# Optimization experiments

Measured on AMD Instinct MI355X. Metric: run time of the kernel, lower is better.

Reference implementation:

```python
import jax, jax.numpy as jnp
import numpy as np

D_MODEL = 1024
N_HEADS = 16
L = 2048
S = 2048
B = 4


def setup_inputs() -> dict:
    key = jax.random.key(0)
    ks = jax.random.split(key, 12)
    std = 0.02
    inp = {
        "query": jax.random.normal(ks[0], (L, B, D_MODEL), dtype=jnp.float32),
        "key": jax.random.normal(ks[1], (S, B, D_MODEL), dtype=jnp.float32),
        "value": jax.random.normal(ks[2], (S, B, D_MODEL), dtype=jnp.float32),
        # True = masked (matches torch masked_fill semantics); causal mask
        "attn_mask": jnp.triu(jnp.ones((L, S), dtype=bool), k=1),
        "Wq": std * jax.random.normal(ks[3], (D_MODEL, D_MODEL), dtype=jnp.float32),
        "bq": jnp.zeros((D_MODEL,), dtype=jnp.float32),
        "Wk": std * jax.random.normal(ks[4], (D_MODEL, D_MODEL), dtype=jnp.float32),
        "bk": jnp.zeros((D_MODEL,), dtype=jnp.float32),
        "Wv": std * jax.random.normal(ks[5], (D_MODEL, D_MODEL), dtype=jnp.float32),
        "bv": jnp.zeros((D_MODEL,), dtype=jnp.float32),
        "Wo": std * jax.random.normal(ks[6], (D_MODEL, D_MODEL), dtype=jnp.float32),
        "bo": jnp.zeros((D_MODEL,), dtype=jnp.float32),
    }
    return inp


def reference(query, key, value, attn_mask, Wq, bq, Wk, bk, Wv, bv, Wo, bo):
    Lq, Bb, D = query.shape
    H = N_HEADS
    dh = D // H
    # NOTE: module uses d_model**-0.5 (not d_qkv**-0.5)
    scale = D ** (-0.5)
    Q = (query @ Wq.T + bq).reshape(Lq, Bb, H, dh)
    K = (key @ Wk.T + bk).reshape(-1, Bb, H, dh)
    V = (value @ Wv.T + bv).reshape(-1, Bb, H, dh)
    # scores: (L, S, B, H)
    scores = jnp.einsum('ibnd,jbnd->ijbn', Q, K) * scale
    scores = jnp.where(attn_mask[:, :, None, None], -jnp.inf, scores)
    attn_weights = jax.nn.softmax(scores, axis=1)  # softmax over key axis j
    # dropout in eval mode -> identity
    out = jnp.einsum('ijbn,jbnd->ibnd', attn_weights, V).reshape(Lq, Bb, D)
    out = out @ Wo.T + bo
    return out
```

## Files before the change

kernel.cpp:

```cpp
#include <hip/hip_runtime.h>
#include <hip/hip_bf16.h>

typedef __hip_bfloat16 bf16;
typedef __attribute__((ext_vector_type(8))) short short8;
typedef __attribute__((ext_vector_type(8))) __bf16 bf16x8;
typedef __attribute__((ext_vector_type(4))) float f32x4;
typedef __attribute__((ext_vector_type(2))) unsigned int u32x2;

#define L_CTX 2048
#define B_SZ 4
#define DM 1024
#define NH 16
#define DH 64
#define M_ROWS (L_CTX * B_SZ)
#define SCQ 0.04508422002778011f

__device__ __forceinline__ void load_lds16(const void* g, void* l) {
  __builtin_amdgcn_global_load_lds(
      (const __attribute__((address_space(1))) unsigned int*)g,
      (__attribute__((address_space(3))) unsigned int*)l, 16, 0, 0);
}

__device__ __forceinline__ f32x4 mfma16(short8 a, short8 b, f32x4 c) {
  return __builtin_amdgcn_mfma_f32_16x16x32_bf16(
      __builtin_bit_cast(bf16x8, a), __builtin_bit_cast(bf16x8, b), c, 0, 0, 0);
}

__device__ __forceinline__ short tobf(float x) {
  return __builtin_bit_cast(short, __float2bfloat16(x));
}

__device__ __forceinline__ short tobf_rh(float x) {
  unsigned u = __builtin_bit_cast(unsigned, x);
  return (short)((u + 0x8000u) >> 16);
}

#if __has_builtin(__builtin_amdgcn_exp2f)
#define EXP2(x) __builtin_amdgcn_exp2f(x)
#else
#define EXP2(x) exp2f(x)
#endif

#if __has_builtin(__builtin_amdgcn_rcpf)
#define RCP(x) __builtin_amdgcn_rcpf(x)
#else
#define RCP(x) (1.0f / (x))
#endif

#define TRRD(d, N) \
  asm volatile("ds_read_b64_tr_b16 %0, %1 offset:" #N : "=v"(d) : "v"(va))

__device__ __forceinline__ short8 mkv(u32x2 a, u32x2 b) {
  union { unsigned u[4]; short8 s; } x;
  x.u[0] = a.x; x.u[1] = a.y; x.u[2] = b.x; x.u[3] = b.y;
  return x.s;
}

__global__ void cast_all(const float* __restrict__ q, const float* __restrict__ k,
                         const float* __restrict__ v, const float* __restrict__ wq,
                         const float* __restrict__ wk, const float* __restrict__ wv,
                         const float* __restrict__ wo, bf16* __restrict__ dq,
                         bf16* __restrict__ dk, bf16* __restrict__ dv,
                         bf16* __restrict__ dwq, bf16* __restrict__ dwk,
                         bf16* __restrict__ dwv, bf16* __restrict__ dwo) {
  unsigned u = blockIdx.x * 256u + threadIdx.x;
  const float* src;
  bf16* dst;
  unsigned off;
  if (u < 3145728u) {
    unsigned which = u >> 20;
    off = u & 1048575u;
    src = which == 0 ? q : which == 1 ? k : v;
    dst = which == 0 ? dq : which == 1 ? dk : dv;
  } else {
    unsigned w = u - 3145728u;
    unsigned which = w >> 17;
    off = w & 131071u;
    src = which == 0 ? wq : which == 1 ? wk : which == 2 ? wv : wo;
    dst = which == 0 ? dwq : which == 1 ? dwk : which == 2 ? dwv : dwo;
  }
  const float4* s4 = (const float4*)src + (size_t)off * 2;
  float4 a = s4[0], b = s4[1];
  union { bf16 h[8]; short8 s; } o;
  o.h[0] = __float2bfloat16(a.x); o.h[1] = __float2bfloat16(a.y);
  o.h[2] = __float2bfloat16(a.z); o.h[3] = __float2bfloat16(a.w);
  o.h[4] = __float2bfloat16(b.x); o.h[5] = __float2bfloat16(b.y);
  o.h[6] = __float2bfloat16(b.z); o.h[7] = __float2bfloat16(b.w);
  *(short8*)(dst + (size_t)off * 8) = o.s;
}

__global__ __launch_bounds__(512, 2) void gemm_qkv(
    const bf16* __restrict__ Aq, const bf16* __restrict__ Ak,
    const bf16* __restrict__ Av, const bf16* __restrict__ Wq,
    const bf16* __restrict__ Wk, const bf16* __restrict__ Wv,
    const float* __restrict__ bq, const float* __restrict__ bk,
    const float* __restrict__ bv, bf16* __restrict__ Oq, bf16* __restrict__ Ok,
    bf16* __restrict__ Ov) {
  const int K = DM;
  int bid = blockIdx.x;
  int xcd = bid & 7, t_ = bid >> 3;
  int z = t_ >> 4, rem = t_ & 15;
  int bx = rem & 3, by = xcd * 4 + (rem >> 2);
  const bf16* A = z == 0 ? Aq : z == 1 ? Ak : Av;
  const bf16* W = z == 0 ? Wq : z == 1 ? Wk : Wv;
  const float* bias = z == 0 ? bq : z == 1 ? bk : bv;
  bf16* Cout = z == 0 ? Oq : z == 1 ? Ok : Ov;
  const float scale = z == 0 ? SCQ : 1.0f;

  const int tid = threadIdx.x;
  const int wid = tid >> 6, ln = tid & 63, g = ln >> 4, lc = ln & 15;
  const int wm = wid >> 2, wn = wid & 3;
  const int bm = by * 256, bn = bx * 256;

  __shared__ char smem[65536];

  f32x4 acc[8][4] = {};

  auto stage = [&](int t, int s) {
    int kk = t * 32;
#pragma unroll
    for (int l = 0; l < 4; ++l) {
      int idx = (l & 1) * 512 + tid;
      int rowi = idx >> 2, chunk = idx & 3;
      int cs = chunk ^ ((rowi >> 1) & 3);
      char* dst = smem + s * 32768 + (l >> 1) * 16384 + (l & 1) * 8192 +
                  wid * 1024 + ln * 16;
      if (l < 2)
        load_lds16(A + (size_t)(bm + rowi) * K + kk + cs * 8, dst);
      else
        load_lds16(W + (size_t)(bn + rowi) * K + kk + cs * 8, dst);
    }
  };

  stage(0, 0);
  asm volatile("s_waitcnt vmcnt(0)" ::: "memory");
  __syncthreads();

  for (int t = 0; t < 32; ++t) {
    if (t + 1 < 32) stage(t + 1, (t + 1) & 1);
    const char* As = smem + (t & 1) * 32768;
    const char* Bs = As + 16384;
    short8 af[8], bfr[4];
#pragma unroll
    for (int m = 0; m < 8; ++m) {
      int row = wm * 128 + m * 16 + lc;
      af[m] = *(const short8*)(As + row * 64 + ((g ^ ((row >> 1) & 3)) << 4));
    }
#pragma unroll
    for (int n = 0; n < 4; ++n) {
      int row = wn * 64 + n * 16 + lc;
      bfr[n] = *(const short8*)(Bs + row * 64 + ((g ^ ((row >> 1) & 3)) << 4));
    }
    __builtin_amdgcn_s_setprio(1);
#pragma unroll
    for (int m = 0; m < 8; ++m)
#pragma unroll
      for (int n = 0; n < 4; ++n) acc[m][n] = mfma16(af[m], bfr[n], acc[m][n]);
    __builtin_amdgcn_s_setprio(0);
    asm volatile("s_waitcnt vmcnt(0)" ::: "memory");
    __syncthreads();
  }

#pragma unroll
  for (int n = 0; n < 4; ++n) {
    int col = bn + wn * 64 + n * 16 + lc;
    float bv = bias[col];
    int h = col >> 6, d = col & 63;
#pragma unroll
    for (int m = 0; m < 8; ++m) {
      int row0 = bm + wm * 128 + m * 16 + g * 4;
#pragma unroll
      for (int i = 0; i < 4; ++i) {
        int row = row0 + i;
        int l = row >> 2, b = row & 3;
        Cout[(((size_t)(b * NH + h)) * L_CTX + l) * DH + d] =
            __float2bfloat16((acc[m][n][i] + bv) * scale);
      }
    }
  }
}

__global__ __launch_bounds__(256, 3) void gemm_out(const bf16* __restrict__ A,
                                                   const bf16* __restrict__ Bw,
                                                   const float* __restrict__ bias,
                                                   float* __restrict__ Cout) {
  const int K = DM, N = DM;
  int bid = blockIdx.x;
  int xcd = bid & 7, t_ = bid >> 3;
  int u = t_ >> 3, bxi = t_ & 7;
  int byi = xcd * 8 + u;
  const int tid = threadIdx.x;
  const int wv = tid >> 6, ln = tid & 63, g = ln >> 4, lc = ln & 15;
  const int wr = wv >> 1, wc = wv & 1;
  const int bm = byi * 128, bn = bxi * 128;

  __shared__ char smem[49152];

  f32x4 acc[4][4] = {};

  const int srow = tid >> 2, sc_ = tid & 3;
  auto stage = [&](int t, int s) {
    int kk = t * 32;
#pragma unroll
    for (int i = 0; i < 2; ++i) {
      int row = i * 64 + srow;
      int cs = sc_ ^ ((row >> 1) & 3);
      load_lds16(A + (size_t)(bm + row) * K + kk + cs * 8,
                 smem + s * 16384 + i * 4096 + wv * 1024);
      load_lds16(Bw + (size_t)(bn + row) * K + kk + cs * 8,
                 smem + s * 16384 + 8192 + i * 4096 + wv * 1024);
    }
  };

  stage(0, 0);
  stage(1, 1);
  asm volatile("s_waitcnt vmcnt(4)" ::: "memory");
  __syncthreads();

#pragma unroll
  for (int t = 0; t < 32; ++t) {
    if (t + 2 < 32) stage(t + 2, (t + 2) % 3);
    const char* As = smem + (t % 3) * 16384;
    const char* Bs = As + 8192;
    short8 af[4], bfr[4];
#pragma unroll
    for (int m = 0; m < 4; ++m) {
      int row = wr * 64 + m * 16 + lc;
      af[m] = *(const short8*)(As + row * 64 + ((g ^ ((row >> 1) & 3)) << 4));
    }
#pragma unroll
    for (int n = 0; n < 4; ++n) {
      int row = wc * 64 + n * 16 + lc;
      bfr[n] = *(const short8*)(Bs + row * 64 + ((g ^ ((row >> 1) & 3)) << 4));
    }
    __builtin_amdgcn_s_setprio(1);
#pragma unroll
    for (int m = 0; m < 4; ++m)
#pragma unroll
      for (int n = 0; n < 4; ++n) acc[m][n] = mfma16(af[m], bfr[n], acc[m][n]);
    __builtin_amdgcn_s_setprio(0);
    if (t + 2 < 32)
      asm volatile("s_waitcnt vmcnt(4)" ::: "memory");
    else
      asm volatile("s_waitcnt vmcnt(0)" ::: "memory");
    __syncthreads();
  }

#pragma unroll
  for (int n = 0; n < 4; ++n) {
    int col = bn + wc * 64 + n * 16 + lc;
    float bv = bias[col];
#pragma unroll
    for (int m = 0; m < 4; ++m) {
      int row0 = bm + wr * 64 + m * 16 + g * 4;
#pragma unroll
      for (int i = 0; i < 4; ++i) {
        int row = row0 + i;
        Cout[(size_t)row * N + col] = acc[m][n][i] + bv;
      }
    }
  }
}

__global__ __launch_bounds__(256, 4) void attn_fwd7(const bf16* __restrict__ Q,
                                                    const bf16* __restrict__ K,
                                                    const bf16* __restrict__ V,
                                                    bf16* __restrict__ O) {
  const int tid = threadIdx.x, w = tid >> 6, ln = tid & 63, g = ln >> 4,
            lc = ln & 15;
  const int bid = blockIdx.x;
  const int j = bid >> 3;
  const int bh = (bid & 7) * 8 + (j & 7);
  const int pa = j >> 3;
  const int b = bh >> 4, h = bh & 15;

  __shared__ char smem[32768];
  const bf16* Qh = Q + (size_t)bh * L_CTX * DH;
  const bf16* Kh = K + (size_t)bh * L_CTX * DH;
  const bf16* Vh = V + (size_t)bh * L_CTX * DH;

  const unsigned vbase =
      (unsigned)(size_t)(__attribute__((address_space(3))) char*)(smem + 16384);

  const int krow_l = ln >> 3, kslot = ln & 7;
  const int vr = (ln & 7) >> 1, vc0 = (ln & 1) * 8;

  const short ONEBF = 0x3F80;
  const short8 ones8 = {ONEBF, ONEBF, ONEBF, ONEBF, ONEBF, ONEBF, ONEBF, ONEBF};

#pragma unroll 1
  for (int rep = 0; rep < 2; ++rep) {
    const int qt = rep ? (31 - pa) : pa;
    const int qb = qt * 64 + w * 16;
    const int nt = qt + 1;

    short8 qf0 = *(const short8*)(Qh + (qb + lc) * DH + g * 8);
    short8 qf1 = *(const short8*)(Qh + (qb + lc) * DH + 32 + g * 8);

    f32x4 oacc[4] = {};
    f32x4 lacc = {};

    auto stage = [&](int t, int s) {
#pragma unroll
      for (int i = 0; i < 2; ++i) {
        int row = (i * 4 + w) * 8 + krow_l;
        int slot = kslot ^ (row & 7);
        load_lds16(Kh + (size_t)(t * 64 + row) * DH + slot * 8,
                   smem + s * 8192 + (i * 4 + w) * 1024);
      }
#pragma unroll
      for (int Lg = 0; Lg < 2; ++Lg) {
        int blk = w * 8 + Lg * 32 + krow_l;
        int sq = blk & 15, dt = blk >> 4;
        load_lds16(Vh + (size_t)(t * 64 + sq * 4 + vr) * DH + dt * 16 + vc0,
                   smem + 16384 + s * 8192 + Lg * 4096 + w * 1024);
      }
    };

    int sel = 0;
    stage(0, 0);
    asm volatile("s_waitcnt vmcnt(0)" ::: "memory");
    __syncthreads();

    for (int t = 0; t < nt; ++t) {
      if (t + 1 < nt) stage(t + 1, sel ^ 1);

      const char* Kl = smem + sel * 8192;
      f32x4 st[4] = {};
      __builtin_amdgcn_s_setprio(1);
#pragma unroll
      for (int tt = 0; tt < 4; ++tt) {
        int row = tt * 16 + lc, sw = lc & 7;
        short8 kf0 = *(const short8*)(Kl + row * 128 + ((g ^ sw) << 4));
        short8 kf1 = *(const short8*)(Kl + row * 128 + (((4 + g) ^ sw) << 4));
        st[tt] = mfma16(kf0, qf0, st[tt]);
        st[tt] = mfma16(kf1, qf1, st[tt]);
      }
      __builtin_amdgcn_s_setprio(0);

      unsigned va = vbase + sel * 8192 + ln * 8;
      u32x2 t0a, t0b, t1a, t1b, t2a, t2b, t3a, t3b;
      u32x2 s0a, s0b, s1a, s1b, s2a, s2b, s3a, s3b;
      TRRD(t0a, 0);    TRRD(t0b, 512);
      TRRD(t1a, 2048); TRRD(t1b, 2560);
      TRRD(t2a, 4096); TRRD(t2b, 4608);
      TRRD(t3a, 6144); TRRD(t3b, 6656);
      TRRD(s0a, 1024); TRRD(s0b, 1536);
      TRRD(s1a, 3072); TRRD(s1b, 3584);
      TRRD(s2a, 5120); TRRD(s2b, 5632);
      TRRD(s3a, 7168); TRRD(s3b, 7680);

      if (t == nt - 1) {
        int qrel = w * 16 + lc;
#pragma unroll
        for (int tt = 0; tt < 4; ++tt)
#pragma unroll
          for (int i = 0; i < 4; ++i)
            if (tt * 16 + g * 4 + i > qrel) st[tt][i] = -__builtin_inff();
      }

      union { short s[8]; short8 v; } p0, p1;
#pragma unroll
      for (int i = 0; i < 4; ++i) {
        p0.s[i]     = tobf_rh(EXP2(st[0][i]));
        p0.s[4 + i] = tobf_rh(EXP2(st[1][i]));
        p1.s[i]     = tobf_rh(EXP2(st[2][i]));
        p1.s[4 + i] = tobf_rh(EXP2(st[3][i]));
      }

      asm volatile("s_waitcnt lgkmcnt(0)" ::: "memory");
      __builtin_amdgcn_sched_barrier(0);
      __builtin_amdgcn_s_setprio(1);
      oacc[0] = mfma16(p0.v, mkv(t0a, t0b), oacc[0]);
      oacc[1] = mfma16(p0.v, mkv(t1a, t1b), oacc[1]);
      oacc[2] = mfma16(p0.v, mkv(t2a, t2b), oacc[2]);
      oacc[3] = mfma16(p0.v, mkv(t3a, t3b), oacc[3]);
      lacc = mfma16(p0.v, ones8, lacc);
      oacc[0] = mfma16(p1.v, mkv(s0a, s0b), oacc[0]);
      oacc[1] = mfma16(p1.v, mkv(s1a, s1b), oacc[1]);
      oacc[2] = mfma16(p1.v, mkv(s2a, s2b), oacc[2]);
      oacc[3] = mfma16(p1.v, mkv(s3a, s3b), oacc[3]);
      lacc = mfma16(p1.v, ones8, lacc);
      __builtin_amdgcn_s_setprio(0);

      asm volatile("s_waitcnt vmcnt(0)" ::: "memory");
      __syncthreads();
      sel ^= 1;
    }

    float li[4];
#pragma unroll
    for (int i = 0; i < 4; ++i) li[i] = RCP(lacc[i]);
#pragma unroll
    for (int n = 0; n < 4; ++n)
#pragma unroll
      for (int i = 0; i < 4; ++i) {
        int qi = qb + g * 4 + i;
        int col = h * DH + n * 16 + lc;
        O[((size_t)qi * B_SZ + b) * DM + col] =
            __float2bfloat16(oacc[n][i] * li[i]);
      }
  }
}

extern "C" void kernel_launch(void* const* d_in, const int* in_sizes, int n_in,
                              void* d_out, int out_size, void* d_ws, size_t ws_size,
                              hipStream_t stream) {
  const float* q = (const float*)d_in[0];
  const float* k = (const float*)d_in[1];
  const float* v = (const float*)d_in[2];
  const float* wq = (const float*)d_in[4];
  const float* bq = (const float*)d_in[5];
  const float* wk = (const float*)d_in[6];
  const float* bk = (const float*)d_in[7];
  const float* wv = (const float*)d_in[8];
  const float* bv = (const float*)d_in[9];
  const float* wo = (const float*)d_in[10];
  const float* bo = (const float*)d_in[11];

  if (ws_size < 125829120u) return;

  char* ws = (char*)d_ws;
  bf16* qb_ = (bf16*)(ws);
  bf16* kb_ = (bf16*)(ws + 16777216);
  bf16* vb_ = (bf16*)(ws + 33554432);
  bf16* wqb = (bf16*)(ws + 50331648);
  bf16* wkb = (bf16*)(ws + 52428800);
  bf16* wvb = (bf16*)(ws + 54525952);
  bf16* wob = (bf16*)(ws + 56623104);
  bf16* Qp = (bf16*)(ws + 58720256);
  bf16* Kp = (bf16*)(ws + 75497472);
  bf16* Vp = (bf16*)(ws + 92274688);
  bf16* Ob = (bf16*)(ws + 109051904);

  cast_all<<<14336, 256, 0, stream>>>(q, k, v, wq, wk, wv, wo, qb_, kb_, vb_, wqb,
                                      wkb, wvb, wob);
  gemm_qkv<<<384, 512, 0, stream>>>(qb_, kb_, vb_, wqb, wkb, wvb, bq, bk, bv,
                                    Qp, Kp, Vp);
  attn_fwd7<<<1024, 256, 0, stream>>>(Qp, Kp, Vp, Ob);
  gemm_out<<<512, 256, 0, stream>>>(Ob, wob, bo, (float*)d_out);
}
```

Baseline: 166.1 us.

## Retile QKV GEMM to 128x256 blocks with triple-buffered LDS pipeline

The QKV projection GEMM drops from 512-thread 256x256 tiles to 256-thread 128x256 tiles, doubling the grid to 768 blocks. The LDS ring grows from two stages to three, so each iteration prefetches two k-steps ahead and waits with a partial vmcnt instead of draining all outstanding loads. The aim is to hide global-load latency and to fill the GPU with more blocks. In exchange, more LDS is used per block and each weight tile is re-read by twice as many blocks.

Measured after the change: 155.3 us. 6.5% less time.

```diff
diff --git a/kernel.cpp b/kernel.cpp
--- a/kernel.cpp
+++ b/kernel.cpp
@@ -89,7 +89,7 @@
   *(short8*)(dst + (size_t)off * 8) = o.s;
 }
 
-__global__ __launch_bounds__(512, 2) void gemm_qkv(
+__global__ __launch_bounds__(256, 2) void gemm_qkv(
     const bf16* __restrict__ Aq, const bf16* __restrict__ Ak,
     const bf16* __restrict__ Av, const bf16* __restrict__ Wq,
     const bf16* __restrict__ Wk, const bf16* __restrict__ Wv,
@@ -99,8 +99,8 @@
   const int K = DM;
   int bid = blockIdx.x;
   int xcd = bid & 7, t_ = bid >> 3;
-  int z = t_ >> 4, rem = t_ & 15;
-  int bx = rem & 3, by = xcd * 4 + (rem >> 2);
+  int z = t_ >> 5, rem = t_ & 31;
+  int bx = rem & 3, by = xcd * 8 + (rem >> 2);
   const bf16* A = z == 0 ? Aq : z == 1 ? Ak : Av;
   const bf16* W = z == 0 ? Wq : z == 1 ? Wk : Wv;
   const float* bias = z == 0 ? bq : z == 1 ? bk : bv;
@@ -108,42 +108,47 @@
   const float scale = z == 0 ? SCQ : 1.0f;
 
   const int tid = threadIdx.x;
-  const int wid = tid >> 6, ln = tid & 63, g = ln >> 4, lc = ln & 15;
-  const int wm = wid >> 2, wn = wid & 3;
-  const int bm = by * 256, bn = bx * 256;
-
-  __shared__ char smem[65536];
+  const int wn = tid >> 6, ln = tid & 63, g = ln >> 4, lc = ln & 15;
+  const int bm = by * 128, bn = bx * 256;
+
+  __shared__ char smem[73728];
 
   f32x4 acc[8][4] = {};
 
   auto stage = [&](int t, int s) {
     int kk = t * 32;
-#pragma unroll
-    for (int l = 0; l < 4; ++l) {
-      int idx = (l & 1) * 512 + tid;
+    char* base = smem + s * 24576;
+#pragma unroll
+    for (int l = 0; l < 2; ++l) {
+      int idx = l * 256 + tid;
       int rowi = idx >> 2, chunk = idx & 3;
       int cs = chunk ^ ((rowi >> 1) & 3);
-      char* dst = smem + s * 32768 + (l >> 1) * 16384 + (l & 1) * 8192 +
-                  wid * 1024 + ln * 16;
-      if (l < 2)
-        load_lds16(A + (size_t)(bm + rowi) * K + kk + cs * 8, dst);
-      else
-        load_lds16(W + (size_t)(bn + rowi) * K + kk + cs * 8, dst);
+      load_lds16(A + (size_t)(bm + rowi) * K + kk + cs * 8, base + idx * 16);
+    }
+#pragma unroll
+    for (int l = 0; l < 4; ++l) {
+      int idx = l * 256 + tid;
+      int rowi = idx >> 2, chunk = idx & 3;
+      int cs = chunk ^ ((rowi >> 1) & 3);
+      load_lds16(W + (size_t)(bn + rowi) * K + kk + cs * 8,
+                 base + 8192 + idx * 16);
     }
   };
 
   stage(0, 0);
-  asm volatile("s_waitcnt vmcnt(0)" ::: "memory");
+  stage(1, 1);
+  asm volatile("s_waitcnt vmcnt(6)" ::: "memory");
   __syncthreads();
 
+#pragma unroll
   for (int t = 0; t < 32; ++t) {
-    if (t + 1 < 32) stage(t + 1, (t + 1) & 1);
-    const char* As = smem + (t & 1) * 32768;
-    const char* Bs = As + 16384;
+    if (t + 2 < 32) stage(t + 2, (t + 2) % 3);
+    const char* As = smem + (t % 3) * 24576;
+    const char* Bs = As + 8192;
     short8 af[8], bfr[4];
 #pragma unroll
     for (int m = 0; m < 8; ++m) {
-      int row = wm * 128 + m * 16 + lc;
+      int row = m * 16 + lc;
       af[m] = *(const short8*)(As + row * 64 + ((g ^ ((row >> 1) & 3)) << 4));
     }
 #pragma unroll
@@ -157,7 +162,10 @@
 #pragma unroll
       for (int n = 0; n < 4; ++n) acc[m][n] = mfma16(af[m], bfr[n], acc[m][n]);
     __builtin_amdgcn_s_setprio(0);
-    asm volatile("s_waitcnt vmcnt(0)" ::: "memory");
+    if (t + 2 < 32)
+      asm volatile("s_waitcnt vmcnt(6)" ::: "memory");
+    else
+      asm volatile("s_waitcnt vmcnt(0)" ::: "memory");
     __syncthreads();
   }
 
@@ -168,7 +176,7 @@
     int h = col >> 6, d = col & 63;
 #pragma unroll
     for (int m = 0; m < 8; ++m) {
-      int row0 = bm + wm * 128 + m * 16 + g * 4;
+      int row0 = bm + m * 16 + g * 4;
 #pragma unroll
       for (int i = 0; i < 4; ++i) {
         int row = row0 + i;
@@ -435,7 +443,7 @@
 
   cast_all<<<14336, 256, 0, stream>>>(q, k, v, wq, wk, wv, wo, qb_, kb_, vb_, wqb,
                                       wkb, wvb, wob);
-  gemm_qkv<<<384, 512, 0, stream>>>(qb_, kb_, vb_, wqb, wkb, wvb, bq, bk, bv,
+  gemm_qkv<<<768, 256, 0, stream>>>(qb_, kb_, vb_, wqb, wkb, wvb, bq, bk, bv,
                                     Qp, Kp, Vp);
   attn_fwd7<<<1024, 256, 0, stream>>>(Qp, Kp, Vp, Ob);
   gemm_out<<<512, 256, 0, stream>>>(Ob, wob, bo, (float*)d_out);
```
